# Performance work log

Hardware: AMD Instinct MI355X
Metric: run time of the kernel (lower is better)

## Reference

```python
import jax, jax.numpy as jnp
import numpy as np

EMBED = 256      # input_size
DOWN = 64        # expert hidden_size
NUM_EXPERTS = 10
TOPK = 2
GATE_SCALE = 0.5
LOSS_COEF = 1.0
CV_EPS = 1e-10


def setup_inputs() -> dict:
    key = jax.random.key(0)
    ks = jax.random.split(key, 6)
    B, N = 16, 4096
    x = jax.random.normal(ks[0], (B, N, EMBED), jnp.float32)
    # gating weight (Parameter in torch; random here so top-k is non-degenerate)
    w_gate = jax.random.normal(ks[1], (EMBED, NUM_EXPERTS), jnp.float32) * 0.02
    # expert MLP params: fc1 (EMBED->DOWN), relu, fc2 (DOWN->EMBED)
    w1 = jax.random.normal(ks[2], (NUM_EXPERTS, EMBED, DOWN), jnp.float32) * (1.0 / np.sqrt(EMBED))
    b1 = jnp.zeros((NUM_EXPERTS, DOWN), jnp.float32)
    w2 = jax.random.normal(ks[3], (NUM_EXPERTS, DOWN, EMBED), jnp.float32) * (1.0 / np.sqrt(DOWN))
    b2 = jnp.zeros((NUM_EXPERTS, EMBED), jnp.float32)
    return {"x": x, "w_gate": w_gate, "w1": w1, "b1": b1, "w2": w2, "b2": b2}


def _cv_squared(v):
    # torch: x.var() / (x.mean()**2 + eps), unbiased variance
    return jnp.var(v, ddof=1) / (jnp.mean(v) ** 2 + CV_EPS)


def reference(x, w_gate, w1, b1, w2, b2):
    B, N, D = x.shape
    xt = x.reshape(B * N, D)                      # (T, D)
    T = B * N

    # --- noisy top-k gating (eval mode: no noise) ---
    logits = xt @ w_gate                          # (T, E)
    top_logits, top_idx = jax.lax.top_k(logits, TOPK)
    top_gates = jax.nn.softmax(top_logits, axis=-1)
    gates = jnp.zeros((T, NUM_EXPERTS), x.dtype).at[
        jnp.arange(T)[:, None], top_idx].set(top_gates)   # (T, E), sparse rows

    importance = gates.sum(axis=0)                               # (E,)
    load = jnp.sum(gates > 0, axis=0).astype(x.dtype)            # (E,)
    aux_loss = (_cv_squared(importance) + _cv_squared(load)) * LOSS_COEF

    # --- expert FFN dispatch+combine (dense equivalent: zero gates kill terms) ---
    h = jax.nn.relu(jnp.einsum('td,edh->teh', xt, w1) + b1[None])   # (T, E, DOWN)
    ye = jnp.einsum('teh,eho->teo', h, w2) + b2[None]               # (T, E, D)
    y = jnp.einsum('te,teo->to', gates, ye)                         # (T, D)

    out = y.reshape(B, N, -1)
    # self-KD L1 loss vs zeros, computed BEFORE gate_scale is applied
    kd_loss = jnp.mean(jnp.abs(out))
    moe_loss = aux_loss + kd_loss
    return out * GATE_SCALE, moe_loss
```

## Files before the change

kernel.cpp:

```cpp
#include <hip/hip_runtime.h>
#include <hip/hip_bf16.h>

#define T_TOKENS 65536
#define EMBED 256
#define DOWN 64
#define NE 10
#define NPAIR 100
#define MAXQ 1280
#define XROW 72

typedef __attribute__((ext_vector_type(8))) short short8;
typedef __attribute__((ext_vector_type(4))) float f32x4;

__device__ inline unsigned short f2bf(float f) {
    unsigned u = __builtin_bit_cast(unsigned, f);
    u += 0x7fff + ((u >> 16) & 1);
    return (unsigned short)(u >> 16);
}
__device__ inline float bf2f(unsigned short h) {
    unsigned u = ((unsigned)h) << 16;
    return __builtin_bit_cast(float, u);
}

__global__ __launch_bounds__(256) void pack_kernel(
    const float* __restrict__ w1, const float* __restrict__ w2,
    unsigned short* __restrict__ w1ph, unsigned short* __restrict__ w1pl,
    unsigned short* __restrict__ w2ph, unsigned short* __restrict__ w2pl)
{
    int gid = blockIdx.x * 256 + threadIdx.x;
    int lane = gid & 63;
    int fid = gid >> 6;
    int n16 = lane & 15;
    int kbase = ((lane >> 4) & 3) * 8;
    if (fid < 320) {
        int kb = fid & 7, ect = fid >> 3;
        int ct = ect & 3, e = ect >> 2;
        int n = ct * 16 + n16;
        int k0 = kb * 32 + kbase;
#pragma unroll
        for (int j = 0; j < 8; ++j) {
            float v = w1[((size_t)e * EMBED + k0 + j) * DOWN + n];
            unsigned short h = f2bf(v);
            w1ph[(size_t)fid * 512 + lane * 8 + j] = h;
            w1pl[(size_t)fid * 512 + lane * 8 + j] = f2bf(v - bf2f(h));
        }
    } else if (fid < 640) {
        int f2 = fid - 320;
        int kb = f2 & 1, ect = f2 >> 1;
        int ct = ect & 15, e = ect >> 4;
        int n = ct * 16 + n16;
        int k0 = kb * 32 + kbase;
#pragma unroll
        for (int j = 0; j < 8; ++j) {
            float v = w2[((size_t)e * DOWN + k0 + j) * EMBED + n];
            unsigned short h = f2bf(v);
            w2ph[(size_t)f2 * 512 + lane * 8 + j] = h;
            w2pl[(size_t)f2 * 512 + lane * 8 + j] = f2bf(v - bf2f(h));
        }
    }
}

__global__ __launch_bounds__(256) void gating_kernel(
    const float* __restrict__ x, const float* __restrict__ wg,
    int* __restrict__ pcount, float* __restrict__ importance,
    int* __restrict__ btok, float* __restrict__ bg0)
{
    __shared__ float Xs[2][256 * 33];
    __shared__ int lcount[NPAIR];
    __shared__ int gbase[NPAIR];
    __shared__ float limp[16];
    int tid = threadIdx.x;
    if (tid < NPAIR) lcount[tid] = 0;
    if (tid < 16) limp[tid] = 0.f;

    int tokbase = blockIdx.x * 256;
    const float4* x4 = (const float4*)x;
    int rbase = tid >> 3, c4 = tid & 7;

    float4 pre[8];
#pragma unroll
    for (int i = 0; i < 8; ++i)
        pre[i] = x4[(size_t)(tokbase + i * 32 + rbase) * 64 + c4];

    float acc[NE];
#pragma unroll
    for (int e = 0; e < NE; e++) acc[e] = 0.f;

    for (int cc = 0; cc < 8; ++cc) {
        float* buf = Xs[cc & 1];
#pragma unroll
        for (int i = 0; i < 8; ++i) {
            float* d = &buf[(i * 32 + rbase) * 33 + c4 * 4];
            d[0] = pre[i].x; d[1] = pre[i].y; d[2] = pre[i].z; d[3] = pre[i].w;
        }
        if (cc < 7) {
#pragma unroll
            for (int i = 0; i < 8; ++i)
                pre[i] = x4[(size_t)(tokbase + i * 32 + rbase) * 64 + (cc + 1) * 8 + c4];
        }
        __syncthreads();
        const float* wgc = wg + cc * 32 * NE;
#pragma unroll
        for (int c = 0; c < 32; ++c) {
            float xv = buf[tid * 33 + c];
#pragma unroll
            for (int e = 0; e < NE; ++e)
                acc[e] = fmaf(xv, wgc[c * NE + e], acc[e]);
        }
    }

    float l0 = -INFINITY, l1 = -INFINITY;
    int i0 = 0, i1 = 0;
#pragma unroll
    for (int e = 0; e < NE; e++) {
        float v = acc[e];
        if (v > l0) { l1 = l0; i1 = i0; l0 = v; i0 = e; }
        else if (v > l1) { l1 = v; i1 = e; }
    }
    float ex = __expf(l1 - l0);
    float g0 = 1.f / (1.f + ex);

    int p = i0 * NE + i1;
    int lp = atomicAdd(&lcount[p], 1);
    atomicAdd(&limp[i0], g0);
    atomicAdd(&limp[i1], 1.f - g0);
    __syncthreads();
    if (tid < NPAIR) {
        int c = lcount[tid];
        gbase[tid] = c ? atomicAdd(&pcount[tid], c) : 0;
    }
    if (tid < NE) atomicAdd(&importance[tid], limp[tid]);
    __syncthreads();
    int pos = gbase[p] + lp;
    btok[p * T_TOKENS + pos] = tokbase + tid;
    bg0[p * T_TOKENS + pos] = g0;
}

__global__ void queue_kernel(const int* __restrict__ pcount,
                             int* __restrict__ qp, int* __restrict__ qs, int* __restrict__ nq)
{
    if (threadIdx.x == 0) {
        int n = 0;
        for (int p = 0; p < NPAIR; p++) {
            int c = pcount[p];
            for (int s = 0; s < c; s += 64) { qp[n] = p; qs[n] = s; n++; }
        }
        *nq = n;
    }
}

__global__ __launch_bounds__(256, 3) void expert_kernel(
    const float* __restrict__ x,
    const unsigned short* __restrict__ w1ph, const unsigned short* __restrict__ w1pl,
    const unsigned short* __restrict__ w2ph, const unsigned short* __restrict__ w2pl,
    const float* __restrict__ b1, const float* __restrict__ b2,
    const int* __restrict__ pcount, const int* __restrict__ qp, const int* __restrict__ qs,
    const int* __restrict__ nq,
    const int* __restrict__ btok, const float* __restrict__ bg0,
    float* __restrict__ out, float* __restrict__ kdpart)
{
    int bid = blockIdx.x;
    if (bid >= *nq) return;
    int p = qp[bid], s = qs[bid];
    int e0 = p / NE, e1 = p - e0 * NE;
    int m = min(64, pcount[p] - s);

    __shared__ __align__(16) unsigned short Xh[64 * XROW], Xl[64 * XROW];
    __shared__ __align__(16) unsigned short H0h[4096], H0l[4096];
    __shared__ __align__(16) unsigned short H1h[4096], H1l[4096];
    __shared__ int toks[64];
    __shared__ float gv0s[64], gv1s[64];
    __shared__ float kdw[4];

    int tid = threadIdx.x;
    if (tid < 64) {
        int v = 0; float g = 0.f;
        if (tid < m) {
            v = btok[p * T_TOKENS + s + tid];
            g = bg0[p * T_TOKENS + s + tid];
        }
        toks[tid] = v;
        gv0s[tid] = g;
        gv1s[tid] = (tid < m) ? (1.f - g) : 0.f;
    }
    __syncthreads();

    int lane = tid & 63, wv = tid >> 6;
    int ln15 = lane & 15, quad = lane >> 4;
    int srow = tid >> 2, sc0 = (tid & 3) * 16;
    const float* xrow = x + (size_t)toks[srow] * EMBED;
    bool srow_ok = srow < m;

    f32x4 a10[4], a11[4];
#pragma unroll
    for (int rt = 0; rt < 4; ++rt) { a10[rt] = (f32x4){0,0,0,0}; a11[rt] = (f32x4){0,0,0,0}; }

    const unsigned short* w1h0 = w1ph + (((size_t)e0 * 4 + wv) * 8) * 512;
    const unsigned short* w1l0 = w1pl + (((size_t)e0 * 4 + wv) * 8) * 512;
    const unsigned short* w1h1 = w1ph + (((size_t)e1 * 4 + wv) * 8) * 512;
    const unsigned short* w1l1 = w1pl + (((size_t)e1 * 4 + wv) * 8) * 512;

    for (int cc = 0; cc < 4; ++cc) {
#pragma unroll
        for (int p4 = 0; p4 < 4; ++p4) {
            int col = sc0 + p4 * 4;
            float4 v = make_float4(0.f, 0.f, 0.f, 0.f);
            if (srow_ok) v = *(const float4*)(xrow + cc * 64 + col);
            const float* vs = (const float*)&v;
            ushort4 hv, lv;
            unsigned short* hp = (unsigned short*)&hv;
            unsigned short* lp2 = (unsigned short*)&lv;
#pragma unroll
            for (int i = 0; i < 4; ++i) {
                unsigned short h = f2bf(vs[i]);
                hp[i] = h;
                lp2[i] = f2bf(vs[i] - bf2f(h));
            }
            *(ushort4*)&Xh[srow * XROW + col] = hv;
            *(ushort4*)&Xl[srow * XROW + col] = lv;
        }
        __syncthreads();
#pragma unroll
        for (int kb = 0; kb < 2; ++kb) {
            int kbg = cc * 2 + kb;
            short8 bh0 = *(const short8*)(w1h0 + (size_t)kbg * 512 + lane * 8);
            short8 bl0 = *(const short8*)(w1l0 + (size_t)kbg * 512 + lane * 8);
            short8 bh1 = *(const short8*)(w1h1 + (size_t)kbg * 512 + lane * 8);
            short8 bl1 = *(const short8*)(w1l1 + (size_t)kbg * 512 + lane * 8);
            int aoff = kb * 32 + quad * 8;
#pragma unroll
            for (int rt = 0; rt < 4; ++rt) {
                short8 ah = *(const short8*)&Xh[(rt * 16 + ln15) * XROW + aoff];
                short8 al = *(const short8*)&Xl[(rt * 16 + ln15) * XROW + aoff];
                a10[rt] = __builtin_amdgcn_mfma_f32_16x16x32_bf16(ah, bh0, a10[rt], 0, 0, 0);
                a10[rt] = __builtin_amdgcn_mfma_f32_16x16x32_bf16(ah, bl0, a10[rt], 0, 0, 0);
                a10[rt] = __builtin_amdgcn_mfma_f32_16x16x32_bf16(al, bh0, a10[rt], 0, 0, 0);
                a11[rt] = __builtin_amdgcn_mfma_f32_16x16x32_bf16(ah, bh1, a11[rt], 0, 0, 0);
                a11[rt] = __builtin_amdgcn_mfma_f32_16x16x32_bf16(ah, bl1, a11[rt], 0, 0, 0);
                a11[rt] = __builtin_amdgcn_mfma_f32_16x16x32_bf16(al, bh1, a11[rt], 0, 0, 0);
            }
        }
        __syncthreads();
    }

    {
        float b1v0 = b1[e0 * DOWN + wv * 16 + ln15];
        float b1v1 = b1[e1 * DOWN + wv * 16 + ln15];
        int kbH = wv >> 1;
        int laneH = (((wv & 1) * 2 + (ln15 >> 3)) * 16) + quad * 4;
        int jH = ln15 & 7;
#pragma unroll
        for (int rt = 0; rt < 4; ++rt) {
#pragma unroll
            for (int r = 0; r < 4; ++r) {
                int row = rt * 16 + quad * 4 + r;
                float g0 = gv0s[row], g1 = gv1s[row];
                float h0 = fmaxf(a10[rt][r] + b1v0, 0.f) * g0;
                float h1 = fmaxf(a11[rt][r] + b1v1, 0.f) * g1;
                int idx = ((rt * 2 + kbH) * 64 + laneH + r) * 8 + jH;
                unsigned short h0h = f2bf(h0);
                unsigned short h1h = f2bf(h1);
                H0h[idx] = h0h; H0l[idx] = f2bf(h0 - bf2f(h0h));
                H1h[idx] = h1h; H1l[idx] = f2bf(h1 - bf2f(h1h));
            }
        }
    }
    __syncthreads();

    float b20[4], b21[4];
#pragma unroll
    for (int ci = 0; ci < 4; ++ci) {
        b20[ci] = b2[e0 * EMBED + (wv * 4 + ci) * 16 + ln15];
        b21[ci] = b2[e1 * EMBED + (wv * 4 + ci) * 16 + ln15];
    }
    float kdacc = 0.f;
#pragma unroll
    for (int rt = 0; rt < 4; ++rt) {
        short8 ah0[2], al0[2], ah1[2], al1[2];
#pragma unroll
        for (int kb = 0; kb < 2; ++kb) {
            int base = ((rt * 2 + kb) * 64 + lane) * 8;
            ah0[kb] = *(const short8*)&H0h[base];
            al0[kb] = *(const short8*)&H0l[base];
            ah1[kb] = *(const short8*)&H1h[base];
            al1[kb] = *(const short8*)&H1l[base];
        }
        int rowb = rt * 16 + quad * 4;
        float gr0[4], gr1[4];
#pragma unroll
        for (int r = 0; r < 4; ++r) { gr0[r] = gv0s[rowb + r]; gr1[r] = gv1s[rowb + r]; }
#pragma unroll
        for (int ci = 0; ci < 4; ++ci) {
            int ct = wv * 4 + ci;
            const unsigned short* p0h = w2ph + (((size_t)e0 * 16 + ct) * 2) * 512;
            const unsigned short* p0l = w2pl + (((size_t)e0 * 16 + ct) * 2) * 512;
            const unsigned short* p1h = w2ph + (((size_t)e1 * 16 + ct) * 2) * 512;
            const unsigned short* p1l = w2pl + (((size_t)e1 * 16 + ct) * 2) * 512;
            f32x4 acc = (f32x4){0, 0, 0, 0};
#pragma unroll
            for (int kb = 0; kb < 2; ++kb) {
                short8 bh = *(const short8*)(p0h + kb * 512 + lane * 8);
                short8 bl = *(const short8*)(p0l + kb * 512 + lane * 8);
                acc = __builtin_amdgcn_mfma_f32_16x16x32_bf16(ah0[kb], bh, acc, 0, 0, 0);
                acc = __builtin_amdgcn_mfma_f32_16x16x32_bf16(ah0[kb], bl, acc, 0, 0, 0);
                acc = __builtin_amdgcn_mfma_f32_16x16x32_bf16(al0[kb], bh, acc, 0, 0, 0);
                short8 ch = *(const short8*)(p1h + kb * 512 + lane * 8);
                short8 cl = *(const short8*)(p1l + kb * 512 + lane * 8);
                acc = __builtin_amdgcn_mfma_f32_16x16x32_bf16(ah1[kb], ch, acc, 0, 0, 0);
                acc = __builtin_amdgcn_mfma_f32_16x16x32_bf16(ah1[kb], cl, acc, 0, 0, 0);
                acc = __builtin_amdgcn_mfma_f32_16x16x32_bf16(al1[kb], ch, acc, 0, 0, 0);
            }
#pragma unroll
            for (int r = 0; r < 4; ++r) {
                int row = rowb + r;
                float val = acc[r] + gr0[r] * b20[ci] + gr1[r] * b21[ci];
                if (row < m) {
                    kdacc += fabsf(val);
                    out[(size_t)toks[row] * EMBED + ct * 16 + ln15] = 0.5f * val;
                }
            }
        }
    }
#pragma unroll
    for (int o = 32; o > 0; o >>= 1) kdacc += __shfl_down(kdacc, o, 64);
    if (lane == 0) kdw[wv] = kdacc;
    __syncthreads();
    if (tid == 0)
        atomicAdd(&kdpart[bid & 63], kdw[0] + kdw[1] + kdw[2] + kdw[3]);
}

__global__ void loss_kernel(const int* __restrict__ pcount, const float* __restrict__ importance,
                            const float* __restrict__ kdpart, float* __restrict__ loss_out)
{
    if (threadIdx.x == 0) {
        float kd = 0.f;
        for (int i = 0; i < 64; i++) kd += kdpart[i];
        kd *= (1.f / (float)((size_t)T_TOKENS * EMBED));
        float load[NE];
        for (int e = 0; e < NE; e++) load[e] = 0.f;
        for (int p = 0; p < NPAIR; p++) {
            float c = (float)pcount[p];
            load[p / NE] += c;
            load[p % NE] += c;
        }
        float mi = 0.f, ml = 0.f;
        for (int e = 0; e < NE; e++) { mi += importance[e]; ml += load[e]; }
        mi *= (1.f / NE); ml *= (1.f / NE);
        float vi = 0.f, vl = 0.f;
        for (int e = 0; e < NE; e++) {
            float di = importance[e] - mi; vi += di * di;
            float dl = load[e] - ml; vl += dl * dl;
        }
        vi *= (1.f / (NE - 1)); vl *= (1.f / (NE - 1));
        float aux = vi / (mi * mi + 1e-10f) + vl / (ml * ml + 1e-10f);
        loss_out[0] = aux + kd;
    }
}

extern "C" void kernel_launch(void* const* d_in, const int* in_sizes, int n_in,
                              void* d_out, int out_size, void* d_ws, size_t ws_size,
                              hipStream_t stream)
{
    (void)in_sizes; (void)n_in; (void)out_size; (void)ws_size;
    const float* x  = (const float*)d_in[0];
    const float* wg = (const float*)d_in[1];
    const float* w1 = (const float*)d_in[2];
    const float* b1 = (const float*)d_in[3];
    const float* w2 = (const float*)d_in[4];
    const float* b2 = (const float*)d_in[5];
    float* out = (float*)d_out;

    char* ws = (char*)d_ws;
    int*   pcount     = (int*)ws;
    float* importance = (float*)(ws + 512);
    float* kdpart     = (float*)(ws + 576);
    int*   nq         = (int*)(ws + 832);
    int*   qp         = (int*)(ws + 1024);
    int*   qs         = (int*)(ws + 1024 + MAXQ * 4);
    size_t off = 16384;
    int*   btok = (int*)(ws + off);    off += (size_t)NPAIR * T_TOKENS * 4;
    float* bg0  = (float*)(ws + off);  off += (size_t)NPAIR * T_TOKENS * 4;
    unsigned short* w1ph = (unsigned short*)(ws + off); off += 327680;
    unsigned short* w1pl = (unsigned short*)(ws + off); off += 327680;
    unsigned short* w2ph = (unsigned short*)(ws + off); off += 327680;
    unsigned short* w2pl = (unsigned short*)(ws + off); off += 327680;

    hipMemsetAsync(ws, 0, 1024, stream);

    pack_kernel<<<160, 256, 0, stream>>>(w1, w2, w1ph, w1pl, w2ph, w2pl);
    gating_kernel<<<T_TOKENS / 256, 256, 0, stream>>>(x, wg, pcount, importance, btok, bg0);
    queue_kernel<<<1, 64, 0, stream>>>(pcount, qp, qs, nq);
    expert_kernel<<<1114, 256, 0, stream>>>(
        x, w1ph, w1pl, w2ph, w2pl, b1, b2, pcount, qp, qs, nq, btok, bg0, out, kdpart);
    loss_kernel<<<1, 64, 0, stream>>>(pcount, importance, kdpart, out + (size_t)T_TOKENS * EMBED);
}
```

Measured before the change: 261.3 us.

## Persistent expert kernel with aliased LDS, parallel queue scan, and deeper gating prefetch

Converts the expert kernel to a grid-stride persistent loop over 1024 blocks and aliases the X staging buffers into the H buffers, cutting LDS use so occupancy can rise to 4 blocks per SIMD. It also register-prefetches the next x chunk before the first GEMM's MFMA work. The serial single-thread queue builder becomes a parallel prefix scan, the loss kernel uses parallel reductions, and gating prefetches two chunks ahead. Risks are higher register pressure at the tighter launch bound and an extra barrier per chunk that the LDS aliasing requires.

```diff
diff --git a/kernel.cpp b/kernel.cpp
--- a/kernel.cpp
+++ b/kernel.cpp
@@ -77,35 +77,62 @@
     const float4* x4 = (const float4*)x;
     int rbase = tid >> 3, c4 = tid & 7;
 
-    float4 pre[8];
+    float4 pre0[8], pre1[8];
 #pragma unroll
     for (int i = 0; i < 8; ++i)
-        pre[i] = x4[(size_t)(tokbase + i * 32 + rbase) * 64 + c4];
+        pre0[i] = x4[(size_t)(tokbase + i * 32 + rbase) * 64 + c4];
+#pragma unroll
+    for (int i = 0; i < 8; ++i)
+        pre1[i] = x4[(size_t)(tokbase + i * 32 + rbase) * 64 + 8 + c4];
 
     float acc[NE];
 #pragma unroll
     for (int e = 0; e < NE; e++) acc[e] = 0.f;
 
-    for (int cc = 0; cc < 8; ++cc) {
-        float* buf = Xs[cc & 1];
-#pragma unroll
-        for (int i = 0; i < 8; ++i) {
-            float* d = &buf[(i * 32 + rbase) * 33 + c4 * 4];
-            d[0] = pre[i].x; d[1] = pre[i].y; d[2] = pre[i].z; d[3] = pre[i].w;
-        }
-        if (cc < 7) {
-#pragma unroll
-            for (int i = 0; i < 8; ++i)
-                pre[i] = x4[(size_t)(tokbase + i * 32 + rbase) * 64 + (cc + 1) * 8 + c4];
-        }
-        __syncthreads();
-        const float* wgc = wg + cc * 32 * NE;
-#pragma unroll
-        for (int c = 0; c < 32; ++c) {
-            float xv = buf[tid * 33 + c];
-#pragma unroll
-            for (int e = 0; e < NE; ++e)
-                acc[e] = fmaf(xv, wgc[c * NE + e], acc[e]);
+    for (int cp = 0; cp < 4; ++cp) {
+        {
+            float* buf = Xs[0];
+#pragma unroll
+            for (int i = 0; i < 8; ++i) {
+                float* d = &buf[(i * 32 + rbase) * 33 + c4 * 4];
+                d[0] = pre0[i].x; d[1] = pre0[i].y; d[2] = pre0[i].z; d[3] = pre0[i].w;
+            }
+            if (cp < 3) {
+#pragma unroll
+                for (int i = 0; i < 8; ++i)
+                    pre0[i] = x4[(size_t)(tokbase + i * 32 + rbase) * 64 + (2 * cp + 2) * 8 + c4];
+            }
+            __syncthreads();
+            const float* wgc = wg + (2 * cp) * 32 * NE;
+#pragma unroll
+            for (int c = 0; c < 32; ++c) {
+                float xv = buf[tid * 33 + c];
+#pragma unroll
+                for (int e = 0; e < NE; ++e)
+                    acc[e] = fmaf(xv, wgc[c * NE + e], acc[e]);
+            }
+        }
+        {
+            float* buf = Xs[1];
+#pragma unroll
+            for (int i = 0; i < 8; ++i) {
+                float* d = &buf[(i * 32 + rbase) * 33 + c4 * 4];
+                d[0] = pre1[i].x; d[1] = pre1[i].y; d[2] = pre1[i].z; d[3] = pre1[i].w;
+            }
+            if (cp < 3) {
+#pragma unroll
+                for (int i = 0; i < 8; ++i)
+                    pre1[i] = x4[(size_t)(tokbase + i * 32 + rbase) * 64 + (2 * cp + 3) * 8 + c4];
+            }
+            __syncthreads();
+            const float* wgc = wg + (2 * cp + 1) * 32 * NE;
+#pragma unroll
+            for (int c = 0; c < 32; ++c) {
+                float xv = buf[tid * 33 + c];
+#pragma unroll
+                for (int e = 0; e < NE; ++e)
+                    acc[e] = fmaf(xv, wgc[c * NE + e], acc[e]);
+            }
         }
     }
 
@@ -136,20 +163,30 @@
     bg0[p * T_TOKENS + pos] = g0;
 }
 
-__global__ void queue_kernel(const int* __restrict__ pcount,
+__global__ __launch_bounds__(128) void queue_kernel(const int* __restrict__ pcount,
                              int* __restrict__ qp, int* __restrict__ qs, int* __restrict__ nq)
 {
-    if (threadIdx.x == 0) {
-        int n = 0;
-        for (int p = 0; p < NPAIR; p++) {
-            int c = pcount[p];
-            for (int s = 0; s < c; s += 64) { qp[n] = p; qs[n] = s; n++; }
-        }
-        *nq = n;
-    }
-}
-
-__global__ __launch_bounds__(256, 3) void expert_kernel(
+    __shared__ int sc[2][128];
+    int tid = threadIdx.x;
+    int c = (tid < NPAIR) ? pcount[tid] : 0;
+    int t = (c + 63) >> 6;
+    sc[0][tid] = t;
+    __syncthreads();
+    int cur = 0;
+#pragma unroll
+    for (int o = 1; o < 128; o <<= 1) {
+        int v = sc[cur][tid] + ((tid >= o) ? sc[cur][tid - o] : 0);
+        sc[cur ^ 1][tid] = v;
+        __syncthreads();
+        cur ^= 1;
+    }
+    int incl = sc[cur][tid];
+    int excl = incl - t;
+    if (tid == 127) *nq = incl;
+    for (int i = 0; i < t; ++i) { qp[excl + i] = tid; qs[excl + i] = i * 64; }
+}
+
+__global__ __launch_bounds__(256, 4) void expert_kernel(
     const float* __restrict__ x,
     const unsigned short* __restrict__ w1ph, const unsigned short* __restrict__ w1pl,
     const unsigned short* __restrict__ w2ph, const unsigned short* __restrict__ w2pl,
@@ -159,197 +196,232 @@
     const int* __restrict__ btok, const float* __restrict__ bg0,
     float* __restrict__ out, float* __restrict__ kdpart)
 {
-    int bid = blockIdx.x;
-    if (bid >= *nq) return;
-    int p = qp[bid], s = qs[bid];
-    int e0 = p / NE, e1 = p - e0 * NE;
-    int m = min(64, pcount[p] - s);
-
-    __shared__ __align__(16) unsigned short Xh[64 * XROW], Xl[64 * XROW];
-    __shared__ __align__(16) unsigned short H0h[4096], H0l[4096];
-    __shared__ __align__(16) unsigned short H1h[4096], H1l[4096];
+    __shared__ __align__(16) unsigned short Hbuf[16384];
     __shared__ int toks[64];
     __shared__ float gv0s[64], gv1s[64];
     __shared__ float kdw[4];
 
+    unsigned short* const Xh  = Hbuf;
+    unsigned short* const Xl  = Hbuf + 64 * XROW;
+    unsigned short* const H0h = Hbuf;
+    unsigned short* const H0l = Hbuf + 4096;
+    unsigned short* const H1h = Hbuf + 8192;
+    unsigned short* const H1l = Hbuf + 12288;
+
     int tid = threadIdx.x;
-    if (tid < 64) {
-        int v = 0; float g = 0.f;
-        if (tid < m) {
-            v = btok[p * T_TOKENS + s + tid];
-            g = bg0[p * T_TOKENS + s + tid];
-        }
-        toks[tid] = v;
-        gv0s[tid] = g;
-        gv1s[tid] = (tid < m) ? (1.f - g) : 0.f;
-    }
-    __syncthreads();
-
     int lane = tid & 63, wv = tid >> 6;
     int ln15 = lane & 15, quad = lane >> 4;
     int srow = tid >> 2, sc0 = (tid & 3) * 16;
-    const float* xrow = x + (size_t)toks[srow] * EMBED;
-    bool srow_ok = srow < m;
-
-    f32x4 a10[4], a11[4];
-#pragma unroll
-    for (int rt = 0; rt < 4; ++rt) { a10[rt] = (f32x4){0,0,0,0}; a11[rt] = (f32x4){0,0,0,0}; }
-
-    const unsigned short* w1h0 = w1ph + (((size_t)e0 * 4 + wv) * 8) * 512;
-    const unsigned short* w1l0 = w1pl + (((size_t)e0 * 4 + wv) * 8) * 512;
-    const unsigned short* w1h1 = w1ph + (((size_t)e1 * 4 + wv) * 8) * 512;
-    const unsigned short* w1l1 = w1pl + (((size_t)e1 * 4 + wv) * 8) * 512;
-
-    for (int cc = 0; cc < 4; ++cc) {
+
+    int nqv = *nq;
+    for (int bid = blockIdx.x; bid < nqv; bid += (int)gridDim.x) {
+        int p = qp[bid], s = qs[bid];
+        int e0 = p / NE, e1 = p - e0 * NE;
+        int m = min(64, pcount[p] - s);
+
+        if (tid < 64) {
+            int v = 0; float g = 0.f;
+            if (tid < m) {
+                v = btok[p * T_TOKENS + s + tid];
+                g = bg0[p * T_TOKENS + s + tid];
+            }
+            toks[tid] = v;
+            gv0s[tid] = g;
+            gv1s[tid] = (tid < m) ? (1.f - g) : 0.f;
+        }
+        __syncthreads();
+
+        const float* xrow = x + (size_t)toks[srow] * EMBED;
+        bool srow_ok = srow < m;
+
+        f32x4 a10[4], a11[4];
+#pragma unroll
+        for (int rt = 0; rt < 4; ++rt) { a10[rt] = (f32x4){0,0,0,0}; a11[rt] = (f32x4){0,0,0,0}; }
+
+        const unsigned short* w1h0 = w1ph + (((size_t)e0 * 4 + wv) * 8) * 512;
+        const unsigned short* w1l0 = w1pl + (((size_t)e0 * 4 + wv) * 8) * 512;
+        const unsigned short* w1h1 = w1ph + (((size_t)e1 * 4 + wv) * 8) * 512;
+        const unsigned short* w1l1 = w1pl + (((size_t)e1 * 4 + wv) * 8) * 512;
+
+        float4 v[4];
 #pragma unroll
         for (int p4 = 0; p4 < 4; ++p4) {
-            int col = sc0 + p4 * 4;
-            float4 v = make_float4(0.f, 0.f, 0.f, 0.f);
-            if (srow_ok) v = *(const float4*)(xrow + cc * 64 + col);
-            const float* vs = (const float*)&v;
-            ushort4 hv, lv;
-            unsigned short* hp = (unsigned short*)&hv;
-            unsigned short* lp2 = (unsigned short*)&lv;
-#pragma unroll
-            for (int i = 0; i < 4; ++i) {
-                unsigned short h = f2bf(vs[i]);
-                hp[i] = h;
-                lp2[i] = f2bf(vs[i] - bf2f(h));
-            }
-            *(ushort4*)&Xh[srow * XROW + col] = hv;
-            *(ushort4*)&Xl[srow * XROW + col] = lv;
+            v[p4] = make_float4(0.f, 0.f, 0.f, 0.f);
+            if (srow_ok) v[p4] = *(const float4*)(xrow + sc0 + p4 * 4);
+        }
+
+#pragma unroll
+        for (int cc = 0; cc < 4; ++cc) {
+#pragma unroll
+            for (int p4 = 0; p4 < 4; ++p4) {
+                int col = sc0 + p4 * 4;
+                const float* vs = (const float*)&v[p4];
+                ushort4 hv, lv;
+                unsigned short* hp = (unsigned short*)&hv;
+                unsigned short* lp2 = (unsigned short*)&lv;
+#pragma unroll
+                for (int i = 0; i < 4; ++i) {
+                    unsigned short h = f2bf(vs[i]);
+                    hp[i] = h;
+                    lp2[i] = f2bf(vs[i] - bf2f(h));
+                }
+                *(ushort4*)&Xh[srow * XROW + col] = hv;
+                *(ushort4*)&Xl[srow * XROW + col] = lv;
+            }
+            float4 nv[4];
+            if (cc < 3) {
+#pragma unroll
+                for (int p4 = 0; p4 < 4; ++p4) {
+                    nv[p4] = make_float4(0.f, 0.f, 0.f, 0.f);
+                    if (srow_ok) nv[p4] = *(const float4*)(xrow + (cc + 1) * 64 + sc0 + p4 * 4);
+                }
+            }
+            __syncthreads();
+#pragma unroll
+            for (int kb = 0; kb < 2; ++kb) {
+                int kbg = cc * 2 + kb;
+                short8 bh0 = *(const short8*)(w1h0 + (size_t)kbg * 512 + lane * 8);
+                short8 bl0 = *(const short8*)(w1l0 + (size_t)kbg * 512 + lane * 8);
+                short8 bh1 = *(const short8*)(w1h1 + (size_t)kbg * 512 + lane * 8);
+                short8 bl1 = *(const short8*)(w1l1 + (size_t)kbg * 512 + lane * 8);
+                int aoff = kb * 32 + quad * 8;
+#pragma unroll
+                for (int rt = 0; rt < 4; ++rt) {
+                    short8 ah = *(const short8*)&Xh[(rt * 16 + ln15) * XROW + aoff];
+                    short8 al = *(const short8*)&Xl[(rt * 16 + ln15) * XROW + aoff];
+                    a10[rt] = __builtin_amdgcn_mfma_f32_16x16x32_bf16(ah, bh0, a10[rt], 0, 0, 0);
+                    a10[rt] = __builtin_amdgcn_mfma_f32_16x16x32_bf16(ah, bl0, a10[rt], 0, 0, 0);
+                    a10[rt] = __builtin_amdgcn_mfma_f32_16x16x32_bf16(al, bh0, a10[rt], 0, 0, 0);
+                    a11[rt] = __builtin_amdgcn_mfma_f32_16x16x32_bf16(ah, bh1, a11[rt], 0, 0, 0);
+                    a11[rt] = __builtin_amdgcn_mfma_f32_16x16x32_bf16(ah, bl1, a11[rt], 0, 0, 0);
+                    a11[rt] = __builtin_amdgcn_mfma_f32_16x16x32_bf16(al, bh1, a11[rt], 0, 0, 0);
+                }
+            }
+            __syncthreads();
+            if (cc < 3) {
+#pragma unroll
+                for (int p4 = 0; p4 < 4; ++p4) v[p4] = nv[p4];
+            }
+        }
+
+        {
+            float b1v0 = b1[e0 * DOWN + wv * 16 + ln15];
+            float b1v1 = b1[e1 * DOWN + wv * 16 + ln15];
+            int kbH = wv >> 1;
+            int laneH = (((wv & 1) * 2 + (ln15 >> 3)) * 16) + quad * 4;
+            int jH = ln15 & 7;
+#pragma unroll
+            for (int rt = 0; rt < 4; ++rt) {
+#pragma unroll
+                for (int r = 0; r < 4; ++r) {
+                    int row = rt * 16 + quad * 4 + r;
+                    float g0 = gv0s[row], g1 = gv1s[row];
+                    float h0 = fmaxf(a10[rt][r] + b1v0, 0.f) * g0;
+                    float h1 = fmaxf(a11[rt][r] + b1v1, 0.f) * g1;
+                    int idx = ((rt * 2 + kbH) * 64 + laneH + r) * 8 + jH;
+                    unsigned short h0h = f2bf(h0);
+                    unsigned short h1h = f2bf(h1);
+                    H0h[idx] = h0h; H0l[idx] = f2bf(h0 - bf2f(h0h));
+                    H1h[idx] = h1h; H1l[idx] = f2bf(h1 - bf2f(h1h));
+                }
+            }
         }
         __syncthreads();
-#pragma unroll
-        for (int kb = 0; kb < 2; ++kb) {
-            int kbg = cc * 2 + kb;
-            short8 bh0 = *(const short8*)(w1h0 + (size_t)kbg * 512 + lane * 8);
-            short8 bl0 = *(const short8*)(w1l0 + (size_t)kbg * 512 + lane * 8);
-            short8 bh1 = *(const short8*)(w1h1 + (size_t)kbg * 512 + lane * 8);
-            short8 bl1 = *(const short8*)(w1l1 + (size_t)kbg * 512 + lane * 8);
-            int aoff = kb * 32 + quad * 8;
-#pragma unroll
-            for (int rt = 0; rt < 4; ++rt) {
-                short8 ah = *(const short8*)&Xh[(rt * 16 + ln15) * XROW + aoff];
-                short8 al = *(const short8*)&Xl[(rt * 16 + ln15) * XROW + aoff];
-                a10[rt] = __builtin_amdgcn_mfma_f32_16x16x32_bf16(ah, bh0, a10[rt], 0, 0, 0);
-                a10[rt] = __builtin_amdgcn_mfma_f32_16x16x32_bf16(ah, bl0, a10[rt], 0, 0, 0);
-                a10[rt] = __builtin_amdgcn_mfma_f32_16x16x32_bf16(al, bh0, a10[rt], 0, 0, 0);
-                a11[rt] = __builtin_amdgcn_mfma_f32_16x16x32_bf16(ah, bh1, a11[rt], 0, 0, 0);
-                a11[rt] = __builtin_amdgcn_mfma_f32_16x16x32_bf16(ah, bl1, a11[rt], 0, 0, 0);
-                a11[rt] = __builtin_amdgcn_mfma_f32_16x16x32_bf16(al, bh1, a11[rt], 0, 0, 0);
-            }
-        }
+
+        float b20[4], b21[4];
+#pragma unroll
+        for (int ci = 0; ci < 4; ++ci) {
+            b20[ci] = b2[e0 * EMBED + (wv * 4 + ci) * 16 + ln15];
+            b21[ci] = b2[e1 * EMBED + (wv * 4 + ci) * 16 + ln15];
+        }
+        float kdacc = 0.f;
+#pragma unroll
+        for (int rt = 0; rt < 4; ++rt) {
+            short8 ah0[2], al0[2], ah1[2], al1[2];
+#pragma unroll
+            for (int kb = 0; kb < 2; ++kb) {
+                int base = ((rt * 2 + kb) * 64 + lane) * 8;
+                ah0[kb] = *(const short8*)&H0h[base];
+                al0[kb] = *(const short8*)&H0l[base];
+                ah1[kb] = *(const short8*)&H1h[base];
+                al1[kb] = *(const short8*)&H1l[base];
+            }
+            int rowb = rt * 16 + quad * 4;
+            float gr0[4], gr1[4];
+#pragma unroll
+            for (int r = 0; r < 4; ++r) { gr0[r] = gv0s[rowb + r]; gr1[r] = gv1s[rowb + r]; }
+#pragma unroll
+            for (int ci = 0; ci < 4; ++ci) {
+                int ct = wv * 4 + ci;
+                const unsigned short* p0h = w2ph + (((size_t)e0 * 16 + ct) * 2) * 512;
+                const unsigned short* p0l = w2pl + (((size_t)e0 * 16 + ct) * 2) * 512;
+                const unsigned short* p1h = w2ph + (((size_t)e1 * 16 + ct) * 2) * 512;
+                const unsigned short* p1l = w2pl + (((size_t)e1 * 16 + ct) * 2) * 512;
+                f32x4 acc = (f32x4){0, 0, 0, 0};
+#pragma unroll
+                for (int kb = 0; kb < 2; ++kb) {
+                    short8 bh = *(const short8*)(p0h + kb * 512 + lane * 8);
+                    short8 bl = *(const short8*)(p0l + kb * 512 + lane * 8);
+                    acc = __builtin_amdgcn_mfma_f32_16x16x32_bf16(ah0[kb], bh, acc, 0, 0, 0);
+                    acc = __builtin_amdgcn_mfma_f32_16x16x32_bf16(ah0[kb], bl, acc, 0, 0, 0);
+                    acc = __builtin_amdgcn_mfma_f32_16x16x32_bf16(al0[kb], bh, acc, 0, 0, 0);
+                    short8 ch = *(const short8*)(p1h + kb * 512 + lane * 8);
+                    short8 cl = *(const short8*)(p1l + kb * 512 + lane * 8);
+                    acc = __builtin_amdgcn_mfma_f32_16x16x32_bf16(ah1[kb], ch, acc, 0, 0, 0);
+                    acc = __builtin_amdgcn_mfma_f32_16x16x32_bf16(ah1[kb], cl, acc, 0, 0, 0);
+                    acc = __builtin_amdgcn_mfma_f32_16x16x32_bf16(al1[kb], ch, acc, 0, 0, 0);
+                }
+#pragma unroll
+                for (int r = 0; r < 4; ++r) {
+                    int row = rowb + r;
+                    float val = acc[r] + gr0[r] * b20[ci] + gr1[r] * b21[ci];
+                    if (row < m) {
+                        kdacc += fabsf(val);
+                        out[(size_t)toks[row] * EMBED + ct * 16 + ln15] = 0.5f * val;
+                    }
+                }
+            }
+        }
+#pragma unroll
+        for (int o = 32; o > 0; o >>= 1) kdacc += __shfl_down(kdacc, o, 64);
+        if (lane == 0) kdw[wv] = kdacc;
         __syncthreads();
-    }
-
-    {
-        float b1v0 = b1[e0 * DOWN + wv * 16 + ln15];
-        float b1v1 = b1[e1 * DOWN + wv * 16 + ln15];
-        int kbH = wv >> 1;
-        int laneH = (((wv & 1) * 2 + (ln15 >> 3)) * 16) + quad * 4;
-        int jH = ln15 & 7;
-#pragma unroll
-        for (int rt = 0; rt < 4; ++rt) {
-#pragma unroll
-            for (int r = 0; r < 4; ++r) {
-                int row = rt * 16 + quad * 4 + r;
-                float g0 = gv0s[row], g1 = gv1s[row];
-                float h0 = fmaxf(a10[rt][r] + b1v0, 0.f) * g0;
-                float h1 = fmaxf(a11[rt][r] + b1v1, 0.f) * g1;
-                int idx = ((rt * 2 + kbH) * 64 + laneH + r) * 8 + jH;
-                unsigned short h0h = f2bf(h0);
-                unsigned short h1h = f2bf(h1);
-                H0h[idx] = h0h; H0l[idx] = f2bf(h0 - bf2f(h0h));
-                H1h[idx] = h1h; H1l[idx] = f2bf(h1 - bf2f(h1h));
-            }
-        }
-    }
+        if (tid == 0)
+            atomicAdd(&kdpart[bid & 63], kdw[0] + kdw[1] + kdw[2] + kdw[3]);
+    }
+}
+
+__global__ __launch_bounds__(128) void loss_kernel(const int* __restrict__ pcount,
+                            const float* __restrict__ importance,
+                            const float* __restrict__ kdpart, float* __restrict__ loss_out)
+{
+    __shared__ float sload[NE];
+    __shared__ float simp[NE];
+    __shared__ float skd;
+    int tid = threadIdx.x;
+    if (tid < NE) { sload[tid] = 0.f; simp[tid] = importance[tid]; }
     __syncthreads();
-
-    float b20[4], b21[4];
-#pragma unroll
-    for (int ci = 0; ci < 4; ++ci) {
-        b20[ci] = b2[e0 * EMBED + (wv * 4 + ci) * 16 + ln15];
-        b21[ci] = b2[e1 * EMBED + (wv * 4 + ci) * 16 + ln15];
-    }
-    float kdacc = 0.f;
-#pragma unroll
-    for (int rt = 0; rt < 4; ++rt) {
-        short8 ah0[2], al0[2], ah1[2], al1[2];
-#pragma unroll
-        for (int kb = 0; kb < 2; ++kb) {
-            int base = ((rt * 2 + kb) * 64 + lane) * 8;
-            ah0[kb] = *(const short8*)&H0h[base];
-            al0[kb] = *(const short8*)&H0l[base];
-            ah1[kb] = *(const short8*)&H1h[base];
-            al1[kb] = *(const short8*)&H1l[base];
-        }
-        int rowb = rt * 16 + quad * 4;
-        float gr0[4], gr1[4];
-#pragma unroll
-        for (int r = 0; r < 4; ++r) { gr0[r] = gv0s[rowb + r]; gr1[r] = gv1s[rowb + r]; }
-#pragma unroll
-        for (int ci = 0; ci < 4; ++ci) {
-            int ct = wv * 4 + ci;
-            const unsigned short* p0h = w2ph + (((size_t)e0 * 16 + ct) * 2) * 512;
-            const unsigned short* p0l = w2pl + (((size_t)e0 * 16 + ct) * 2) * 512;
-            const unsigned short* p1h = w2ph + (((size_t)e1 * 16 + ct) * 2) * 512;
-            const unsigned short* p1l = w2pl + (((size_t)e1 * 16 + ct) * 2) * 512;
-            f32x4 acc = (f32x4){0, 0, 0, 0};
-#pragma unroll
-            for (int kb = 0; kb < 2; ++kb) {
-                short8 bh = *(const short8*)(p0h + kb * 512 + lane * 8);
-                short8 bl = *(const short8*)(p0l + kb * 512 + lane * 8);
-                acc = __builtin_amdgcn_mfma_f32_16x16x32_bf16(ah0[kb], bh, acc, 0, 0, 0);
-                acc = __builtin_amdgcn_mfma_f32_16x16x32_bf16(ah0[kb], bl, acc, 0, 0, 0);
-                acc = __builtin_amdgcn_mfma_f32_16x16x32_bf16(al0[kb], bh, acc, 0, 0, 0);
-                short8 ch = *(const short8*)(p1h + kb * 512 + lane * 8);
-                short8 cl = *(const short8*)(p1l + kb * 512 + lane * 8);
-                acc = __builtin_amdgcn_mfma_f32_16x16x32_bf16(ah1[kb], ch, acc, 0, 0, 0);
-                acc = __builtin_amdgcn_mfma_f32_16x16x32_bf16(ah1[kb], cl, acc, 0, 0, 0);
-                acc = __builtin_amdgcn_mfma_f32_16x16x32_bf16(al1[kb], ch, acc, 0, 0, 0);
-            }
-#pragma unroll
-            for (int r = 0; r < 4; ++r) {
-                int row = rowb + r;
-                float val = acc[r] + gr0[r] * b20[ci] + gr1[r] * b21[ci];
-                if (row < m) {
-                    kdacc += fabsf(val);
-                    out[(size_t)toks[row] * EMBED + ct * 16 + ln15] = 0.5f * val;
-                }
-            }
-        }
-    }
-#pragma unroll
-    for (int o = 32; o > 0; o >>= 1) kdacc += __shfl_down(kdacc, o, 64);
-    if (lane == 0) kdw[wv] = kdacc;
+    if (tid < 64) {
+        float kd = kdpart[tid];
+#pragma unroll
+        for (int o = 32; o > 0; o >>= 1) kd += __shfl_down(kd, o, 64);
+        if (tid == 0) skd = kd;
+    }
+    if (tid < NPAIR) {
+        float c = (float)pcount[tid];
+        atomicAdd(&sload[tid / NE], c);
+        atomicAdd(&sload[tid % NE], c);
+    }
     __syncthreads();
-    if (tid == 0)
-        atomicAdd(&kdpart[bid & 63], kdw[0] + kdw[1] + kdw[2] + kdw[3]);
-}
-
-__global__ void loss_kernel(const int* __restrict__ pcount, const float* __restrict__ importance,
-                            const float* __restrict__ kdpart, float* __restrict__ loss_out)
-{
-    if (threadIdx.x == 0) {
-        float kd = 0.f;
-        for (int i = 0; i < 64; i++) kd += kdpart[i];
-        kd *= (1.f / (float)((size_t)T_TOKENS * EMBED));
-        float load[NE];
-        for (int e = 0; e < NE; e++) load[e] = 0.f;
-        for (int p = 0; p < NPAIR; p++) {
-            float c = (float)pcount[p];
-            load[p / NE] += c;
-            load[p % NE] += c;
-        }
+    if (tid == 0) {
+        float kd = skd * (1.f / (float)((size_t)T_TOKENS * EMBED));
         float mi = 0.f, ml = 0.f;
-        for (int e = 0; e < NE; e++) { mi += importance[e]; ml += load[e]; }
+        for (int e = 0; e < NE; e++) { mi += simp[e]; ml += sload[e]; }
         mi *= (1.f / NE); ml *= (1.f / NE);
         float vi = 0.f, vl = 0.f;
         for (int e = 0; e < NE; e++) {
-            float di = importance[e] - mi; vi += di * di;
-            float dl = load[e] - ml; vl += dl * dl;
+            float di = simp[e] - mi; vi += di * di;
+            float dl = sload[e] - ml; vl += dl * dl;
         }
         vi *= (1.f / (NE - 1)); vl *= (1.f / (NE - 1));
         float aux = vi / (mi * mi + 1e-10f) + vl / (ml * ml + 1e-10f);
@@ -389,8 +461,8 @@
 
     pack_kernel<<<160, 256, 0, stream>>>(w1, w2, w1ph, w1pl, w2ph, w2pl);
     gating_kernel<<<T_TOKENS / 256, 256, 0, stream>>>(x, wg, pcount, importance, btok, bg0);
-    queue_kernel<<<1, 64, 0, stream>>>(pcount, qp, qs, nq);
-    expert_kernel<<<1114, 256, 0, stream>>>(
+    queue_kernel<<<1, 128, 0, stream>>>(pcount, qp, qs, nq);
+    expert_kernel<<<1024, 256, 0, stream>>>(
         x, w1ph, w1pl, w2ph, w2pl, b1, b2, pcount, qp, qs, nq, btok, bg0, out, kdpart);
-    loss_kernel<<<1, 64, 0, stream>>>(pcount, importance, kdpart, out + (size_t)T_TOKENS * EMBED);
-}
+    loss_kernel<<<1, 128, 0, stream>>>(pcount, importance, kdpart, out + (size_t)T_TOKENS * EMBED);
+}
```

After: 331.2 us. 1.27x slower.
